# Performance work log

Hardware: AMD Instinct MI355X
Metric: run time of the kernel (lower is better)

## Reference

```python
import jax, jax.numpy as jnp
import numpy as np

T, B, A = 128, 512, 5
X, Y, Z, H, R = 2, 10, 32, 128, 128
LOG2PI = np.float32(np.log(2.0 * np.pi))


def setup_inputs() -> dict:
    key = jax.random.key(0)
    ks = iter(jax.random.split(key, 40))
    w = lambda *s: jax.random.normal(next(ks), s, jnp.float32) * 0.05
    return dict(
        states=jax.random.normal(next(ks), (T, B, Y), jnp.float32),
        eps=jax.random.normal(next(ks), (T - 1, B, A, Z), jnp.float32),
        enc_w1=w(A, X + Y + R, H), enc_b1=w(A, H),
        enc_w2=w(A, H, H), enc_b2=w(A, H),
        enc_mw=w(A, H, Z), enc_mb=w(A, Z),
        enc_sw=w(A, H, Z), enc_sb=w(A, Z),
        pri_w1=w(A, Y + R, H), pri_b1=w(A, H),
        pri_w2=w(A, H, H), pri_b2=w(A, H),
        pri_mw=w(A, H, Z), pri_mb=w(A, Z),
        pri_sw=w(A, H, Z), pri_sb=w(A, Z),
        dec_w1=w(A, Y + Z + R, H), dec_b1=w(A, H),
        dec_w2=w(A, H, H), dec_b2=w(A, H),
        dec_mw=w(A, H, X), dec_mb=w(A, X),
        dec_sw=w(A, H, X), dec_sb=w(A, X),
        gru_wih=w(A, X + Z, 3 * R), gru_whh=w(A, R, 3 * R),
        gru_bih=w(A, 3 * R), gru_bhh=w(A, 3 * R),
    )


def _lin(x, wt, b):
    # x: [B, A, I], wt: [A, I, O] -> [B, A, O]  (per-agent linear)
    return jnp.einsum('bai,aio->bao', x, wt) + b


def _mlp(x, w1, b1, w2, b2):
    return jax.nn.relu(_lin(jax.nn.relu(_lin(x, w1, b1)), w2, b2))


def reference(states, eps, enc_w1, enc_b1, enc_w2, enc_b2, enc_mw, enc_mb,
              enc_sw, enc_sb, pri_w1, pri_b1, pri_w2, pri_b2, pri_mw, pri_mb,
              pri_sw, pri_sb, dec_w1, dec_b1, dec_w2, dec_b2, dec_mw, dec_mb,
              dec_sw, dec_sb, gru_wih, gru_whh, gru_bih, gru_bhh):
    y_all = states[:-1]                              # [T-1, B, Y]
    x_all = states[1:].reshape(T - 1, B, A, X)       # per-agent next positions

    def step(carry, xs):
        h, kl, nll = carry                           # h: [B, A, R]
        y, x, e = xs                                 # y:[B,Y] x:[B,A,X] e:[B,A,Z]
        yb = jnp.broadcast_to(y[:, None, :], (B, A, Y))
        enc_h = _mlp(jnp.concatenate([x, yb, h], -1), enc_w1, enc_b1, enc_w2, enc_b2)
        enc_m = _lin(enc_h, enc_mw, enc_mb)
        enc_s = jax.nn.softplus(_lin(enc_h, enc_sw, enc_sb))
        pri_h = _mlp(jnp.concatenate([yb, h], -1), pri_w1, pri_b1, pri_w2, pri_b2)
        pri_m = _lin(pri_h, pri_mw, pri_mb)
        pri_s = jax.nn.softplus(_lin(pri_h, pri_sw, pri_sb))
        z = enc_m + enc_s * e                         # reparameterized sample
        dec_h = _mlp(jnp.concatenate([yb, z, h], -1), dec_w1, dec_b1, dec_w2, dec_b2)
        dec_m = _lin(dec_h, dec_mw, dec_mb)
        dec_s = jax.nn.softplus(_lin(dec_h, dec_sw, dec_sb))
        # GRU cell (torch gate order: r, z, n)
        gi = _lin(jnp.concatenate([x, z], -1), gru_wih, gru_bih)   # [B,A,3R]
        gh = _lin(h, gru_whh, gru_bhh)
        gir, giz, gin = jnp.split(gi, 3, -1)
        ghr, ghz, ghn = jnp.split(gh, 3, -1)
        r = jax.nn.sigmoid(gir + ghr)
        u = jax.nn.sigmoid(giz + ghz)
        n = jnp.tanh(gin + r * ghn)
        h_new = (1.0 - u) * n + u * h
        kl_t = 0.5 * jnp.sum(2.0 * jnp.log(pri_s) - 2.0 * jnp.log(enc_s)
                             + (enc_s ** 2 + (enc_m - pri_m) ** 2) / pri_s ** 2 - 1.0)
        nll_t = jnp.sum(0.5 * LOG2PI + jnp.log(dec_s) + 0.5 * ((x - dec_m) / dec_s) ** 2)
        return (h_new, kl + kl_t, nll + nll_t), None

    h0 = jnp.zeros((B, A, R), states.dtype)
    zero = jnp.zeros((), states.dtype)
    (h, kl, nll), _ = jax.lax.scan(step, (h0, zero, zero), (y_all, x_all, eps))
    return jnp.stack([kl, nll])  # [kl_loss, recon_loss]
```

## Files before the change

kernel.cpp:

```cpp
#include <hip/hip_runtime.h>

typedef __attribute__((ext_vector_type(8))) short bf16x8;
typedef __attribute__((ext_vector_type(4))) float f32x4;

#define MFMA_B16(A,B,C) __builtin_amdgcn_mfma_f32_16x16x32_bf16((A),(B),(C),0,0,0)

#define FO_ENC1 0
#define FO_PRI1 48
#define FO_DEC1 88
#define FO_GIH  136
#define FO_GHH  184
#define FO_ENC2 280
#define FO_PRI2 312
#define FO_DEC2 344
#define FO_MS   376
#define FO_DECMS 408
#define NFRAG   412

#define MS 264
#define TS 136

__device__ __forceinline__ unsigned short f2bf(float f) {
  union { float f; unsigned u; } v; v.f = f;
  unsigned r = (v.u + 0x7fffu + ((v.u >> 16) & 1u)) >> 16;
  return (unsigned short)r;
}
__device__ __forceinline__ float bf2f(unsigned short h) {
  union { unsigned u; float f; } v; v.u = ((unsigned)h) << 16;
  return v.f;
}
__device__ __forceinline__ float sigm_(float x) { return 1.f / (1.f + __expf(-x)); }
__device__ __forceinline__ float tanh_(float x) {
  x = fminf(fmaxf(x, -15.f), 15.f);
  float e = __expf(-2.f * x);
  return (1.f - e) / (1.f + e);
}
__device__ __forceinline__ float splus_(float x) {
  return fmaxf(x, 0.f) + log1pf(__expf(-fabsf(x)));
}
__device__ __forceinline__ float ldnt(const float* p) {
  return __builtin_nontemporal_load(p);
}

__global__ void prep_kernel(const float* __restrict__ ew1, const float* __restrict__ pw1,
                            const float* __restrict__ dw1, const float* __restrict__ wih,
                            const float* __restrict__ whh, const float* __restrict__ ew2,
                            const float* __restrict__ pw2, const float* __restrict__ dw2,
                            const float* __restrict__ emw, const float* __restrict__ esw,
                            const float* __restrict__ pmw, const float* __restrict__ psw,
                            const float* __restrict__ dmw, const float* __restrict__ dsw,
                            unsigned short* __restrict__ ws)
{
  int blk = blockIdx.x;
  int a = blk / NFRAG, f = blk % NFRAG;
  int l = threadIdx.x, lg = l >> 4, ln = l & 15;
  float v[8];

  if (f < FO_PRI1) {
    int fi = f, nt = fi / 6, kb = fi % 6, n = nt * 16 + ln;
#pragma unroll
    for (int j = 0; j < 8; ++j) {
      int mk = kb * 32 + lg * 8 + j;
      int r = (mk < 2) ? mk : (mk >= 34 && mk < 44) ? 2 + (mk - 34)
            : (mk >= 64) ? 12 + (mk - 64) : -1;
      v[j] = (r >= 0) ? ew1[((size_t)a * 140 + r) * 128 + n] : 0.f;
    }
  } else if (f < FO_DEC1) {
    int fi = f - FO_PRI1, nt = fi / 5, kb = 1 + fi % 5, n = nt * 16 + ln;
#pragma unroll
    for (int j = 0; j < 8; ++j) {
      int mk = kb * 32 + lg * 8 + j;
      int r = (mk >= 34 && mk < 44) ? (mk - 34) : (mk >= 64) ? 10 + (mk - 64) : -1;
      v[j] = (r >= 0) ? pw1[((size_t)a * 138 + r) * 128 + n] : 0.f;
    }
  } else if (f < FO_GIH) {
    int fi = f - FO_DEC1, nt = fi / 6, kb = fi % 6, n = nt * 16 + ln;
#pragma unroll
    for (int j = 0; j < 8; ++j) {
      int mk = kb * 32 + lg * 8 + j;
      int r = (mk >= 2 && mk < 34) ? 10 + (mk - 2) : (mk >= 34 && mk < 44) ? (mk - 34)
            : (mk >= 64) ? 42 + (mk - 64) : -1;
      v[j] = (r >= 0) ? dw1[((size_t)a * 170 + r) * 128 + n] : 0.f;
    }
  } else if (f < FO_GHH) {
    int fi = f - FO_GIH, nt = fi / 2, kb = fi % 2, n = nt * 16 + ln;
#pragma unroll
    for (int j = 0; j < 8; ++j) {
      int mk = kb * 32 + lg * 8 + j;
      v[j] = (mk < 34) ? wih[((size_t)a * 34 + mk) * 384 + n] : 0.f;
    }
  } else if (f < FO_ENC2) {
    int fi = f - FO_GHH, nt = fi / 4, kb = fi % 4, n = nt * 16 + ln;
#pragma unroll
    for (int j = 0; j < 8; ++j) {
      int r = kb * 32 + lg * 8 + j;
      v[j] = whh[((size_t)a * 128 + r) * 384 + n];
    }
  } else if (f < FO_DEC2) {
    int fi = f - FO_ENC2;
    const float* W = (fi < 32) ? ew2 : pw2;
    fi &= 31;
    int nt = fi / 4, kb = fi % 4, n = nt * 16 + ln;
#pragma unroll
    for (int j = 0; j < 8; ++j) {
      int r = kb * 32 + lg * 8 + j;
      v[j] = W[((size_t)a * 128 + r) * 128 + n];
    }
  } else if (f < FO_MS) {
    int fi = f - FO_DEC2, nt = fi / 4, kb = fi % 4, n = nt * 16 + ln;
#pragma unroll
    for (int j = 0; j < 8; ++j) {
      int r = kb * 32 + lg * 8 + j;
      v[j] = dw2[((size_t)a * 128 + r) * 128 + n];
    }
  } else if (f < FO_DECMS) {
    int fi = f - FO_MS, mat = fi / 8, rem = fi % 8, nt = rem / 4, kb = rem % 4;
    int n = nt * 16 + ln;
    const float* W = (mat == 0) ? emw : (mat == 1) ? esw : (mat == 2) ? pmw : psw;
#pragma unroll
    for (int j = 0; j < 8; ++j) {
      int r = kb * 32 + lg * 8 + j;
      v[j] = W[((size_t)a * 128 + r) * 32 + n];
    }
  } else {
    int kb = f - FO_DECMS;
#pragma unroll
    for (int j = 0; j < 8; ++j) {
      int r = kb * 32 + lg * 8 + j;
      v[j] = (ln < 2) ? dmw[((size_t)a * 128 + r) * 2 + ln]
           : (ln < 4) ? dsw[((size_t)a * 128 + r) * 2 + (ln - 2)] : 0.f;
    }
  }
  unsigned short* dst = ws + (size_t)blk * 512 + l * 8;
#pragma unroll
  for (int j = 0; j < 8; ++j) dst[j] = f2bf(v[j]);
}

#define LD_FRAG(idx) (*(const bf16x8*)(fa + (size_t)(idx) * 512 + l * 8))

__global__ __launch_bounds__(256, 1) void vrnn_main(
    const float* __restrict__ states, const float* __restrict__ eps,
    const float* __restrict__ eb1, const float* __restrict__ eb2,
    const float* __restrict__ emb, const float* __restrict__ esb,
    const float* __restrict__ pb1, const float* __restrict__ pb2,
    const float* __restrict__ pmb, const float* __restrict__ psb,
    const float* __restrict__ db1, const float* __restrict__ db2,
    const float* __restrict__ dmb, const float* __restrict__ dsb,
    const float* __restrict__ bih, const float* __restrict__ bhh,
    const unsigned short* __restrict__ frags, float* __restrict__ out)
{
  const int a = blockIdx.y;
  const int b0 = blockIdx.x * 16;
  const int tid = threadIdx.x;
  const int w = tid >> 6, l = tid & 63, lg = l >> 4, ln = l & 15;

  __shared__ __align__(16) unsigned short ghh_lds[96 * 512];
  __shared__ __align__(16) unsigned short dms_lds[4 * 512];
  __shared__ __align__(16) unsigned short master[16 * MS];
  __shared__ __align__(16) unsigned short t1e[16 * TS], t1p[16 * TS];
  __shared__ __align__(16) unsigned short he[16 * TS], hp[16 * TS];
  __shared__ __align__(16) unsigned short t1d[16 * TS], hdbuf[16 * TS];
  __shared__ float msbuf[4][16][32];
  __shared__ float red[8];

  const unsigned short* fa = frags + (size_t)a * NFRAG * 512;

  {
    const uint4* s1 = (const uint4*)(fa + (size_t)FO_GHH * 512);
    uint4* d1 = (uint4*)ghh_lds;
    for (int i = tid; i < 96 * 64; i += 256) d1[i] = s1[i];
    const uint4* s3 = (const uint4*)(fa + (size_t)FO_DECMS * 512);
    uint4* d3 = (uint4*)dms_lds;
    d3[tid] = s3[tid];
  }
  for (int i = tid; i < 16 * MS; i += 256) master[i] = 0;

  float eb1v[2], pb1v[2], eb2v[2], pb2v[2], db2v[2], d1b[2], ghb[3][2];
#pragma unroll
  for (int j = 0; j < 2; ++j) {
    int n = (w + 4 * j) * 16 + ln;
    eb1v[j] = eb1[a * 128 + n]; pb1v[j] = pb1[a * 128 + n];
    eb2v[j] = eb2[a * 128 + n]; pb2v[j] = pb2[a * 128 + n];
    db2v[j] = db2[a * 128 + n]; d1b[j]  = db1[a * 128 + n];
#pragma unroll
    for (int g = 0; g < 3; ++g)
      ghb[g][j] = bih[a * 384 + g * 128 + n] + bhh[a * 384 + g * 128 + n];
  }
  float hbm, hbs, dmsb = 0.f;
  if (w < 2) { hbm = emb[a * 32 + w * 16 + ln]; hbs = esb[a * 32 + w * 16 + ln]; }
  else { hbm = pmb[a * 32 + (w - 2) * 16 + ln]; hbs = psb[a * 32 + (w - 2) * 16 + ln]; }
  if (w == 0) dmsb = (ln < 2) ? dmb[a * 2 + ln] : (ln < 4) ? dsb[a * 2 + (ln - 2)] : 0.f;

  __syncthreads();

  if (tid < 160) {
    int row = tid / 10, c = tid - row * 10;
    master[row * MS + 34 + c] = f2bf(ldnt(states + (size_t)(b0 + row) * 10 + c));
  }
  if (tid >= 192 && tid < 224) {
    int i = tid - 192, row = i >> 1, c = i & 1;
    master[row * MS + c] = f2bf(ldnt(states + ((size_t)512 + b0 + row) * 10 + a * 2 + c));
  }
  float e_cur[4] = {0.f, 0.f, 0.f, 0.f};
  if (w < 2) {
#pragma unroll
    for (int q = 0; q < 4; ++q)
      e_cur[q] = ldnt(eps + ((size_t)(b0 + 4 * lg + q) * 5 + a) * 32 + w * 16 + ln);
  }
  float xv[4] = {0.f, 0.f, 0.f, 0.f};
  float h_reg[2][4];
#pragma unroll
  for (int j = 0; j < 2; ++j)
#pragma unroll
    for (int q = 0; q < 4; ++q) h_reg[j][q] = 0.f;
  float kl = 0.f, nll = 0.f;
  f32x4 gh[3][2];
  __syncthreads();

  for (int t = 0; t < 127; ++t) {
    const int base_t = (t & 1) * 200;
    const int base_n = ((t + 1) & 1) * 200;

    bf16x8 amA[2], am_h[4];
#pragma unroll
    for (int kb = 0; kb < 2; ++kb)
      amA[kb] = *(const bf16x8*)&master[ln * MS + base_t + kb * 32 + lg * 8];
#pragma unroll
    for (int kb = 0; kb < 4; ++kb)
      am_h[kb] = *(const bf16x8*)&master[ln * MS + 64 + kb * 32 + lg * 8];
    {
      bf16x8 f1[12], f2[10];
#pragma unroll
      for (int j = 0; j < 2; ++j) {
#pragma unroll
        for (int kb = 0; kb < 6; ++kb) f1[j * 6 + kb] = LD_FRAG(FO_ENC1 + (w + 4 * j) * 6 + kb);
#pragma unroll
        for (int kb = 0; kb < 5; ++kb) f2[j * 5 + kb] = LD_FRAG(FO_PRI1 + (w + 4 * j) * 5 + kb);
      }
#pragma unroll
      for (int j = 0; j < 2; ++j) {
        f32x4 a1 = {eb1v[j], eb1v[j], eb1v[j], eb1v[j]};
        f32x4 a2 = {pb1v[j], pb1v[j], pb1v[j], pb1v[j]};
#pragma unroll
        for (int kb = 0; kb < 6; ++kb)
          a1 = MFMA_B16(kb < 2 ? amA[kb] : am_h[kb - 2], f1[j * 6 + kb], a1);
#pragma unroll
        for (int i = 0; i < 5; ++i)
          a2 = MFMA_B16(i == 0 ? amA[1] : am_h[i - 1], f2[j * 5 + i], a2);
#pragma unroll
        for (int q = 0; q < 4; ++q) {
          t1e[(4 * lg + q) * TS + (w + 4 * j) * 16 + ln] = f2bf(fmaxf(a1[q], 0.f));
          t1p[(4 * lg + q) * TS + (w + 4 * j) * 16 + ln] = f2bf(fmaxf(a2[q], 0.f));
        }
      }
    }
    __syncthreads();

    {
      bf16x8 g1[8], g2[8];
#pragma unroll
      for (int j = 0; j < 2; ++j)
#pragma unroll
        for (int kb = 0; kb < 4; ++kb) {
          g1[j * 4 + kb] = LD_FRAG(FO_ENC2 + (w + 4 * j) * 4 + kb);
          g2[j * 4 + kb] = LD_FRAG(FO_PRI2 + (w + 4 * j) * 4 + kb);
        }
      bf16x8 ae[4], ap[4];
#pragma unroll
      for (int kb = 0; kb < 4; ++kb) {
        ae[kb] = *(const bf16x8*)&t1e[ln * TS + kb * 32 + lg * 8];
        ap[kb] = *(const bf16x8*)&t1p[ln * TS + kb * 32 + lg * 8];
      }
#pragma unroll
      for (int j = 0; j < 2; ++j) {
        f32x4 a1 = {eb2v[j], eb2v[j], eb2v[j], eb2v[j]};
        f32x4 a2 = {pb2v[j], pb2v[j], pb2v[j], pb2v[j]};
#pragma unroll
        for (int kb = 0; kb < 4; ++kb) {
          a1 = MFMA_B16(ae[kb], g1[j * 4 + kb], a1);
          a2 = MFMA_B16(ap[kb], g2[j * 4 + kb], a2);
        }
#pragma unroll
        for (int q = 0; q < 4; ++q) {
          he[(4 * lg + q) * TS + (w + 4 * j) * 16 + ln] = f2bf(fmaxf(a1[q], 0.f));
          hp[(4 * lg + q) * TS + (w + 4 * j) * 16 + ln] = f2bf(fmaxf(a2[q], 0.f));
        }
      }
#pragma unroll
      for (int g = 0; g < 3; ++g)
#pragma unroll
        for (int j = 0; j < 2; ++j) {
          float bv = ghb[g][j];
          gh[g][j] = (f32x4){bv, bv, bv, bv};
        }
#pragma unroll
      for (int kb = 0; kb < 4; ++kb)
#pragma unroll
        for (int g = 0; g < 3; ++g)
#pragma unroll
          for (int j = 0; j < 2; ++j)
            gh[g][j] = MFMA_B16(am_h[kb],
              *(const bf16x8*)&ghh_lds[(size_t)((g * 8 + w + 4 * j) * 4 + kb) * 512 + l * 8],
              gh[g][j]);
    }
    __syncthreads();

    {
      const unsigned short* hs = (w < 2) ? he : hp;
      int mbase = FO_MS + ((w < 2) ? 0 : 16) + (w & 1) * 4;
      bf16x8 fm[4], fs[4];
#pragma unroll
      for (int kb = 0; kb < 4; ++kb) {
        fm[kb] = LD_FRAG(mbase + kb);
        fs[kb] = LD_FRAG(mbase + 8 + kb);
      }
      bf16x8 ah[4];
#pragma unroll
      for (int kb = 0; kb < 4; ++kb)
        ah[kb] = *(const bf16x8*)&hs[ln * TS + kb * 32 + lg * 8];
      f32x4 m = {hbm, hbm, hbm, hbm}, s = {hbs, hbs, hbs, hbs};
#pragma unroll
      for (int kb = 0; kb < 4; ++kb) {
        m = MFMA_B16(ah[kb], fm[kb], m);
        s = MFMA_B16(ah[kb], fs[kb], s);
      }
      if (w < 2) {
#pragma unroll
        for (int q = 0; q < 4; ++q) {
          float es = splus_(s[q]);
          msbuf[0][4 * lg + q][w * 16 + ln] = m[q];
          msbuf[1][4 * lg + q][w * 16 + ln] = es;
          master[(4 * lg + q) * MS + base_t + 2 + w * 16 + ln] = f2bf(m[q] + es * e_cur[q]);
        }
      } else {
#pragma unroll
        for (int q = 0; q < 4; ++q) {
          msbuf[2][4 * lg + q][(w - 2) * 16 + ln] = m[q];
          msbuf[3][4 * lg + q][(w - 2) * 16 + ln] = splus_(s[q]);
        }
      }
      if (t > 0) {
        bf16x8 fd2[8];
#pragma unroll
        for (int j = 0; j < 2; ++j)
#pragma unroll
          for (int kb = 0; kb < 4; ++kb)
            fd2[j * 4 + kb] = LD_FRAG(FO_DEC2 + (w + 4 * j) * 4 + kb);
        bf16x8 ad[4];
#pragma unroll
        for (int kb = 0; kb < 4; ++kb)
          ad[kb] = *(const bf16x8*)&t1d[ln * TS + kb * 32 + lg * 8];
#pragma unroll
        for (int j = 0; j < 2; ++j) {
          f32x4 acc = {db2v[j], db2v[j], db2v[j], db2v[j]};
#pragma unroll
          for (int kb = 0; kb < 4; ++kb) acc = MFMA_B16(ad[kb], fd2[j * 4 + kb], acc);
#pragma unroll
          for (int q = 0; q < 4; ++q)
            hdbuf[(4 * lg + q) * TS + (w + 4 * j) * 16 + ln] = f2bf(fmaxf(acc[q], 0.f));
        }
      }
      if (t < 126) {
        if (tid < 160) {
          int row = tid / 10, c = tid - row * 10;
          master[row * MS + base_n + 34 + c] =
            f2bf(ldnt(states + ((size_t)(t + 1) * 512 + b0 + row) * 10 + c));
        }
        if (tid >= 192 && tid < 224) {
          int i = tid - 192, row = i >> 1, c = i & 1;
          master[row * MS + base_n + c] =
            f2bf(ldnt(states + ((size_t)(t + 2) * 512 + b0 + row) * 10 + a * 2 + c));
        }
      }
    }
    __syncthreads();

    {
      bf16x8 amZ[2];
#pragma unroll
      for (int kb = 0; kb < 2; ++kb)
        amZ[kb] = *(const bf16x8*)&master[ln * MS + base_t + kb * 32 + lg * 8];
      if (w == 0) {
#pragma unroll
        for (int q = 0; q < 4; ++q)
          xv[q] = ldnt(states + ((size_t)(t + 1) * 512 + b0 + 4 * lg + q) * 10
                       + a * 2 + (ln & 1));
      }
      bf16x8 fd[12], fg[12];
#pragma unroll
      for (int j = 0; j < 2; ++j)
#pragma unroll
        for (int kb = 0; kb < 6; ++kb)
          fd[j * 6 + kb] = LD_FRAG(FO_DEC1 + (w + 4 * j) * 6 + kb);
#pragma unroll
      for (int g = 0; g < 3; ++g)
#pragma unroll
        for (int j = 0; j < 2; ++j)
#pragma unroll
          for (int kb = 0; kb < 2; ++kb)
            fg[g * 4 + j * 2 + kb] = LD_FRAG(FO_GIH + (g * 8 + w + 4 * j) * 2 + kb);

      if (w == 0 && t > 0) {
        f32x4 acc = {dmsb, dmsb, dmsb, dmsb};
#pragma unroll
        for (int kb = 0; kb < 4; ++kb) {
          bf16x8 ad = *(const bf16x8*)&hdbuf[ln * TS + kb * 32 + lg * 8];
          bf16x8 bf = *(const bf16x8*)&dms_lds[kb * 512 + l * 8];
          acc = MFMA_B16(ad, bf, acc);
        }
#pragma unroll
        for (int q = 0; q < 4; ++q) {
          float sv = __shfl(splus_(acc[q]), l + 2);
          if (ln < 2) {
            float d = (xv[q] - acc[q]) / sv;
            nll += 0.9189385332f + __logf(sv) + 0.5f * d * d;
          }
        }
      }

#pragma unroll
      for (int j = 0; j < 2; ++j) {
        f32x4 acc = {d1b[j], d1b[j], d1b[j], d1b[j]};
#pragma unroll
        for (int kb = 0; kb < 6; ++kb)
          acc = MFMA_B16(kb < 2 ? amZ[kb] : am_h[kb - 2], fd[j * 6 + kb], acc);
#pragma unroll
        for (int q = 0; q < 4; ++q)
          t1d[(4 * lg + q) * TS + (w + 4 * j) * 16 + ln] = f2bf(fmaxf(acc[q], 0.f));
      }
      f32x4 gi[3][2];
#pragma unroll
      for (int g = 0; g < 3; ++g)
#pragma unroll
        for (int j = 0; j < 2; ++j) gi[g][j] = (f32x4){0.f, 0.f, 0.f, 0.f};
#pragma unroll
      for (int kb = 0; kb < 2; ++kb)
#pragma unroll
        for (int g = 0; g < 3; ++g)
#pragma unroll
          for (int j = 0; j < 2; ++j)
            gi[g][j] = MFMA_B16(amZ[kb], fg[g * 4 + j * 2 + kb], gi[g][j]);
#pragma unroll
      for (int j = 0; j < 2; ++j)
#pragma unroll
        for (int q = 0; q < 4; ++q) {
          float r_ = sigm_(gi[0][j][q] + gh[0][j][q]);
          float u_ = sigm_(gi[1][j][q] + gh[1][j][q]);
          float n_ = tanh_(gi[2][j][q] + r_ * gh[2][j][q]);
          float hn = (1.f - u_) * n_ + u_ * h_reg[j][q];
          h_reg[j][q] = hn;
          master[(4 * lg + q) * MS + 64 + (w + 4 * j) * 16 + ln] = f2bf(hn);
        }
#pragma unroll
      for (int rr = 0; rr < 2; ++rr) {
        int elem = rr * 64 + l;
        int row = w * 4 + (elem >> 5), col = elem & 31;
        float em_ = msbuf[0][row][col], es_ = msbuf[1][row][col];
        float pm_ = msbuf[2][row][col], ps_ = msbuf[3][row][col];
        float dm = em_ - pm_;
        kl += 0.5f * (2.f * __logf(ps_) - 2.f * __logf(es_)
                      + (es_ * es_ + dm * dm) / (ps_ * ps_) - 1.f);
      }
      if (w < 2 && t < 126) {
#pragma unroll
        for (int q = 0; q < 4; ++q)
          e_cur[q] = ldnt(eps + ((size_t)((t + 1) * 512 + b0 + 4 * lg + q) * 5 + a) * 32
                          + w * 16 + ln);
      }
    }
    __syncthreads();
  }

  {
    bf16x8 fd2[8];
#pragma unroll
    for (int j = 0; j < 2; ++j)
#pragma unroll
      for (int kb = 0; kb < 4; ++kb)
        fd2[j * 4 + kb] = LD_FRAG(FO_DEC2 + (w + 4 * j) * 4 + kb);
    bf16x8 ad[4];
#pragma unroll
    for (int kb = 0; kb < 4; ++kb)
      ad[kb] = *(const bf16x8*)&t1d[ln * TS + kb * 32 + lg * 8];
#pragma unroll
    for (int j = 0; j < 2; ++j) {
      f32x4 acc = {db2v[j], db2v[j], db2v[j], db2v[j]};
#pragma unroll
      for (int kb = 0; kb < 4; ++kb) acc = MFMA_B16(ad[kb], fd2[j * 4 + kb], acc);
#pragma unroll
      for (int q = 0; q < 4; ++q)
        hdbuf[(4 * lg + q) * TS + (w + 4 * j) * 16 + ln] = f2bf(fmaxf(acc[q], 0.f));
    }
  }
  __syncthreads();
  if (w == 0) {
    f32x4 acc = {dmsb, dmsb, dmsb, dmsb};
#pragma unroll
    for (int kb = 0; kb < 4; ++kb) {
      bf16x8 ad = *(const bf16x8*)&hdbuf[ln * TS + kb * 32 + lg * 8];
      bf16x8 bf = *(const bf16x8*)&dms_lds[kb * 512 + l * 8];
      acc = MFMA_B16(ad, bf, acc);
    }
#pragma unroll
    for (int q = 0; q < 4; ++q) {
      float sv = __shfl(splus_(acc[q]), l + 2);
      if (ln < 2) {
        float d = (xv[q] - acc[q]) / sv;
        nll += 0.9189385332f + __logf(sv) + 0.5f * d * d;
      }
    }
  }

#pragma unroll
  for (int off = 32; off > 0; off >>= 1) {
    kl += __shfl_down(kl, off);
    nll += __shfl_down(nll, off);
  }
  if (l == 0) { red[w] = kl; red[4 + w] = nll; }
  __syncthreads();
  if (tid == 0) {
    float K = 0.f, N = 0.f;
#pragma unroll
    for (int i = 0; i < 4; ++i) { K += red[i]; N += red[4 + i]; }
    atomicAdd(out, K);
    atomicAdd(out + 1, N);
  }
}

extern "C" void kernel_launch(void* const* d_in, const int* in_sizes, int n_in,
                              void* d_out, int out_size, void* d_ws, size_t ws_size,
                              hipStream_t stream) {
  (void)in_sizes; (void)n_in; (void)out_size; (void)ws_size;
  const float* states = (const float*)d_in[0];
  const float* eps    = (const float*)d_in[1];
  const float* ew1 = (const float*)d_in[2];
  const float* eb1 = (const float*)d_in[3];
  const float* ew2 = (const float*)d_in[4];
  const float* eb2 = (const float*)d_in[5];
  const float* emw = (const float*)d_in[6];
  const float* emb = (const float*)d_in[7];
  const float* esw = (const float*)d_in[8];
  const float* esb = (const float*)d_in[9];
  const float* pw1 = (const float*)d_in[10];
  const float* pb1 = (const float*)d_in[11];
  const float* pw2 = (const float*)d_in[12];
  const float* pb2 = (const float*)d_in[13];
  const float* pmw = (const float*)d_in[14];
  const float* pmb = (const float*)d_in[15];
  const float* psw = (const float*)d_in[16];
  const float* psb = (const float*)d_in[17];
  const float* dw1 = (const float*)d_in[18];
  const float* db1 = (const float*)d_in[19];
  const float* dw2 = (const float*)d_in[20];
  const float* db2 = (const float*)d_in[21];
  const float* dmw = (const float*)d_in[22];
  const float* dmb = (const float*)d_in[23];
  const float* dsw = (const float*)d_in[24];
  const float* dsb = (const float*)d_in[25];
  const float* wih = (const float*)d_in[26];
  const float* whh = (const float*)d_in[27];
  const float* bih = (const float*)d_in[28];
  const float* bhh = (const float*)d_in[29];

  unsigned short* frags = (unsigned short*)d_ws;
  float* out = (float*)d_out;

  hipMemsetAsync(d_out, 0, 2 * sizeof(float), stream);
  prep_kernel<<<dim3(5 * NFRAG), dim3(64), 0, stream>>>(
      ew1, pw1, dw1, wih, whh, ew2, pw2, dw2, emw, esw, pmw, psw, dmw, dsw, frags);
  vrnn_main<<<dim3(32, 5), dim3(256), 0, stream>>>(
      states, eps, eb1, eb2, emb, esb, pb1, pb2, pmb, psb,
      db1, db2, dmb, dsb, bih, bhh, frags, out);
}
```

Measured before the change: 976.8 us.

## Use hardware bf16 pack conversion, lighter barriers, and prefetch next-step states earlier

Replaces the software round-to-nearest bf16 conversion with the packed v_cvt_pk_bf16_f32 instruction for all LDS activation stores. It swaps __syncthreads for a barrier that waits only on LDS counters (lgkmcnt), so outstanding global loads no longer stall each step. It also issues the next timestep's states/x loads into registers early in the step and moves the xv load later, hiding global latency in the serial recurrence. The rounding of the packed conversion may differ slightly from the manual version, and the custom barrier depends on correct counter semantics.

After: 1.009 ms. 1.03x slower.

```diff
diff --git a/kernel.cpp b/kernel.cpp
--- a/kernel.cpp
+++ b/kernel.cpp
@@ -41,6 +41,24 @@
 __device__ __forceinline__ float ldnt(const float* p) {
   return __builtin_nontemporal_load(p);
 }
+__device__ __forceinline__ void st4bf(unsigned short* base, int stride, f32x4 v) {
+  unsigned r0, r1;
+  asm("v_cvt_pk_bf16_f32 %0, %1, %2" : "=v"(r0) : "v"(v[0]), "v"(v[1]));
+  asm("v_cvt_pk_bf16_f32 %0, %1, %2" : "=v"(r1) : "v"(v[2]), "v"(v[3]));
+  base[0]          = (unsigned short)r0;
+  base[stride]     = (unsigned short)(r0 >> 16);
+  base[2 * stride] = (unsigned short)r1;
+  base[3 * stride] = (unsigned short)(r1 >> 16);
+}
+__device__ __forceinline__ f32x4 relu4(f32x4 v) {
+  f32x4 r;
+#pragma unroll
+  for (int q = 0; q < 4; ++q) r[q] = fmaxf(v[q], 0.f);
+  return r;
+}
+#define SBAR() __builtin_amdgcn_sched_barrier(0)
+#define BARRIER() do { SBAR(); asm volatile("s_waitcnt lgkmcnt(0)"); \
+                       __builtin_amdgcn_s_barrier(); SBAR(); } while (0)
 
 __global__ void prep_kernel(const float* __restrict__ ew1, const float* __restrict__ pw1,
                             const float* __restrict__ dw1, const float* __restrict__ wih,
@@ -195,7 +213,7 @@
 
   if (tid < 160) {
     int row = tid / 10, c = tid - row * 10;
-    master[row * MS + 34 + c] = f2bf(ldnt(states + (size_t)(b0 + row) * 10 + c));
+    master[row * MS + 34 + c] = f2bf(ldnt(states + (size_t)(b0 + row) * 10 + tid - row * 10));
   }
   if (tid >= 192 && tid < 224) {
     int i = tid - 192, row = i >> 1, c = i & 1;
@@ -220,6 +238,7 @@
   for (int t = 0; t < 127; ++t) {
     const int base_t = (t & 1) * 200;
     const int base_n = ((t + 1) & 1) * 200;
+    float yv = 0.f, xvs = 0.f;
 
     bf16x8 amA[2], am_h[4];
 #pragma unroll
@@ -247,16 +266,23 @@
 #pragma unroll
         for (int i = 0; i < 5; ++i)
           a2 = MFMA_B16(i == 0 ? amA[1] : am_h[i - 1], f2[j * 5 + i], a2);
-#pragma unroll
-        for (int q = 0; q < 4; ++q) {
-          t1e[(4 * lg + q) * TS + (w + 4 * j) * 16 + ln] = f2bf(fmaxf(a1[q], 0.f));
-          t1p[(4 * lg + q) * TS + (w + 4 * j) * 16 + ln] = f2bf(fmaxf(a2[q], 0.f));
-        }
-      }
-    }
-    __syncthreads();
+        st4bf(&t1e[(4 * lg) * TS + (w + 4 * j) * 16 + ln], TS, relu4(a1));
+        st4bf(&t1p[(4 * lg) * TS + (w + 4 * j) * 16 + ln], TS, relu4(a2));
+      }
+    }
+    BARRIER();
 
     {
+      if (t < 126) {
+        if (tid < 160) {
+          int row = tid / 10, c = tid - row * 10;
+          yv = ldnt(states + ((size_t)(t + 1) * 512 + b0 + row) * 10 + c);
+        }
+        if (tid >= 192 && tid < 224) {
+          int i = tid - 192;
+          xvs = ldnt(states + ((size_t)(t + 2) * 512 + b0 + (i >> 1)) * 10 + a * 2 + (i & 1));
+        }
+      }
       bf16x8 g1[8], g2[8];
 #pragma unroll
       for (int j = 0; j < 2; ++j)
@@ -280,11 +306,8 @@
           a1 = MFMA_B16(ae[kb], g1[j * 4 + kb], a1);
           a2 = MFMA_B16(ap[kb], g2[j * 4 + kb], a2);
         }
-#pragma unroll
-        for (int q = 0; q < 4; ++q) {
-          he[(4 * lg + q) * TS + (w + 4 * j) * 16 + ln] = f2bf(fmaxf(a1[q], 0.f));
-          hp[(4 * lg + q) * TS + (w + 4 * j) * 16 + ln] = f2bf(fmaxf(a2[q], 0.f));
-        }
+        st4bf(&he[(4 * lg) * TS + (w + 4 * j) * 16 + ln], TS, relu4(a1));
+        st4bf(&hp[(4 * lg) * TS + (w + 4 * j) * 16 + ln], TS, relu4(a2));
       }
 #pragma unroll
       for (int g = 0; g < 3; ++g)
@@ -303,7 +326,7 @@
               *(const bf16x8*)&ghh_lds[(size_t)((g * 8 + w + 4 * j) * 4 + kb) * 512 + l * 8],
               gh[g][j]);
     }
-    __syncthreads();
+    BARRIER();
 
     {
       const unsigned short* hs = (w < 2) ? he : hp;
@@ -325,13 +348,15 @@
         s = MFMA_B16(ah[kb], fs[kb], s);
       }
       if (w < 2) {
+        f32x4 zv;
 #pragma unroll
         for (int q = 0; q < 4; ++q) {
           float es = splus_(s[q]);
           msbuf[0][4 * lg + q][w * 16 + ln] = m[q];
           msbuf[1][4 * lg + q][w * 16 + ln] = es;
-          master[(4 * lg + q) * MS + base_t + 2 + w * 16 + ln] = f2bf(m[q] + es * e_cur[q]);
-        }
+          zv[q] = m[q] + es * e_cur[q];
+        }
+        st4bf(&master[(4 * lg) * MS + base_t + 2 + w * 16 + ln], MS, zv);
       } else {
 #pragma unroll
         for (int q = 0; q < 4; ++q) {
@@ -355,37 +380,27 @@
           f32x4 acc = {db2v[j], db2v[j], db2v[j], db2v[j]};
 #pragma unroll
           for (int kb = 0; kb < 4; ++kb) acc = MFMA_B16(ad[kb], fd2[j * 4 + kb], acc);
-#pragma unroll
-          for (int q = 0; q < 4; ++q)
-            hdbuf[(4 * lg + q) * TS + (w + 4 * j) * 16 + ln] = f2bf(fmaxf(acc[q], 0.f));
+          st4bf(&hdbuf[(4 * lg) * TS + (w + 4 * j) * 16 + ln], TS, relu4(acc));
         }
       }
       if (t < 126) {
         if (tid < 160) {
           int row = tid / 10, c = tid - row * 10;
-          master[row * MS + base_n + 34 + c] =
-            f2bf(ldnt(states + ((size_t)(t + 1) * 512 + b0 + row) * 10 + c));
+          master[row * MS + base_n + 34 + c] = f2bf(yv);
         }
         if (tid >= 192 && tid < 224) {
           int i = tid - 192, row = i >> 1, c = i & 1;
-          master[row * MS + base_n + c] =
-            f2bf(ldnt(states + ((size_t)(t + 2) * 512 + b0 + row) * 10 + a * 2 + c));
-        }
-      }
-    }
-    __syncthreads();
+          master[row * MS + base_n + c] = f2bf(xvs);
+        }
+      }
+    }
+    BARRIER();
 
     {
       bf16x8 amZ[2];
 #pragma unroll
       for (int kb = 0; kb < 2; ++kb)
         amZ[kb] = *(const bf16x8*)&master[ln * MS + base_t + kb * 32 + lg * 8];
-      if (w == 0) {
-#pragma unroll
-        for (int q = 0; q < 4; ++q)
-          xv[q] = ldnt(states + ((size_t)(t + 1) * 512 + b0 + 4 * lg + q) * 10
-                       + a * 2 + (ln & 1));
-      }
       bf16x8 fd[12], fg[12];
 #pragma unroll
       for (int j = 0; j < 2; ++j)
@@ -417,16 +432,19 @@
           }
         }
       }
-
+      if (w == 0) {
+#pragma unroll
+        for (int q = 0; q < 4; ++q)
+          xv[q] = ldnt(states + ((size_t)(t + 1) * 512 + b0 + 4 * lg + q) * 10
+                       + a * 2 + (ln & 1));
+      }
 #pragma unroll
       for (int j = 0; j < 2; ++j) {
         f32x4 acc = {d1b[j], d1b[j], d1b[j], d1b[j]};
 #pragma unroll
         for (int kb = 0; kb < 6; ++kb)
           acc = MFMA_B16(kb < 2 ? amZ[kb] : am_h[kb - 2], fd[j * 6 + kb], acc);
-#pragma unroll
-        for (int q = 0; q < 4; ++q)
-          t1d[(4 * lg + q) * TS + (w + 4 * j) * 16 + ln] = f2bf(fmaxf(acc[q], 0.f));
+        st4bf(&t1d[(4 * lg) * TS + (w + 4 * j) * 16 + ln], TS, relu4(acc));
       }
       f32x4 gi[3][2];
 #pragma unroll
@@ -441,7 +459,8 @@
           for (int j = 0; j < 2; ++j)
             gi[g][j] = MFMA_B16(amZ[kb], fg[g * 4 + j * 2 + kb], gi[g][j]);
 #pragma unroll
-      for (int j = 0; j < 2; ++j)
+      for (int j = 0; j < 2; ++j) {
+        f32x4 hv;
 #pragma unroll
         for (int q = 0; q < 4; ++q) {
           float r_ = sigm_(gi[0][j][q] + gh[0][j][q]);
@@ -449,8 +468,10 @@
           float n_ = tanh_(gi[2][j][q] + r_ * gh[2][j][q]);
           float hn = (1.f - u_) * n_ + u_ * h_reg[j][q];
           h_reg[j][q] = hn;
-          master[(4 * lg + q) * MS + 64 + (w + 4 * j) * 16 + ln] = f2bf(hn);
-        }
+          hv[q] = hn;
+        }
+        st4bf(&master[(4 * lg) * MS + 64 + (w + 4 * j) * 16 + ln], MS, hv);
+      }
 #pragma unroll
       for (int rr = 0; rr < 2; ++rr) {
         int elem = rr * 64 + l;
@@ -468,7 +489,7 @@
                           + w * 16 + ln);
       }
     }
-    __syncthreads();
+    BARRIER();
   }
 
   {
@@ -487,9 +508,7 @@
       f32x4 acc = {db2v[j], db2v[j], db2v[j], db2v[j]};
 #pragma unroll
       for (int kb = 0; kb < 4; ++kb) acc = MFMA_B16(ad[kb], fd2[j * 4 + kb], acc);
-#pragma unroll
-      for (int q = 0; q < 4; ++q)
-        hdbuf[(4 * lg + q) * TS + (w + 4 * j) * 16 + ln] = f2bf(fmaxf(acc[q], 0.f));
+      st4bf(&hdbuf[(4 * lg) * TS + (w + 4 * j) * 16 + ln], TS, relu4(acc));
     }
   }
   __syncthreads();
```
